# Optimization experiments

Hardware: AMD Instinct MI355X
Metric: run time of the kernel (lower is better)

The kernel has to match this reference:

```python
import jax, jax.numpy as jnp
import numpy as np

N_NODES = 100000
N_EDGES = 625000
D_IN = 128
D_OUT = 128


def setup_inputs() -> dict:
    key = jax.random.key(0)
    k1, k2, k3, k4, k5 = jax.random.split(key, 5)
    scale = 1.0 / np.sqrt(D_IN)
    x = jax.random.normal(k1, (N_NODES, D_IN), dtype=jnp.float32)
    edge_index = jax.random.randint(k2, (2, N_EDGES), 0, N_NODES, dtype=jnp.int64)
    W_l = jax.random.normal(k3, (D_IN, D_OUT), dtype=jnp.float32) * scale
    b_l = jax.random.normal(k4, (D_OUT,), dtype=jnp.float32) * scale
    W_r = jax.random.normal(k5, (D_IN, D_OUT), dtype=jnp.float32) * scale
    return {"x": x, "edge_index": edge_index, "W_l": W_l, "b_l": b_l, "W_r": W_r}


def reference(x, edge_index, W_l, b_l, W_r):
    # SAGEConv (mean aggr, no self loops):
    #   out = lin_l(mean_{j in N(i)} x_j) + lin_r(x_i)
    src = edge_index[0]  # message source nodes
    dst = edge_index[1]  # aggregation targets
    n = x.shape[0]
    msgs = x[src]  # [E, D_IN] gather
    agg = jax.ops.segment_sum(msgs, dst, num_segments=n)  # [N, D_IN]
    deg = jax.ops.segment_sum(jnp.ones_like(dst, dtype=x.dtype), dst, num_segments=n)
    mean = agg / jnp.maximum(deg, 1.0)[:, None]  # isolated nodes -> 0
    return mean @ W_l + b_l + x @ W_r
```

## Files before the change

### kernel.cpp

```cpp
#include <hip/hip_runtime.h>


constexpr int N_NODES = 100000;
constexpr int N_EDGES = 625000;
constexpr int D = 128;
constexpr int SCAN_CHUNK = 1024;
constexpr int N_SCAN_BLOCKS = (N_NODES + SCAN_CHUNK - 1) / SCAN_CHUNK;
constexpr int CONV_BLOCKS = N_NODES * D / (512 * 4);
constexpr int ZERO_BLOCKS = (N_NODES / 4 + 255) / 256;
constexpr int E4 = N_EDGES / 4;

typedef __attribute__((ext_vector_type(8))) short short8;
typedef __attribute__((ext_vector_type(4))) short short4v;
typedef __attribute__((ext_vector_type(4))) float f32x4;

__device__ __forceinline__ unsigned short f2bf(float f) {
    union { float f; unsigned int u; } c; c.f = f;
    unsigned int u = c.u + 0x7fffu + ((c.u >> 16) & 1u);
    return (unsigned short)(u >> 16);
}
__device__ __forceinline__ float bflo(unsigned int v) {
    union { unsigned int u; float f; } c; c.u = v << 16; return c.f;
}
__device__ __forceinline__ float bfhi(unsigned int v) {
    union { unsigned int u; float f; } c; c.u = v & 0xffff0000u; return c.f;
}
__device__ __forceinline__ uint2 pack4(float4 a) {
    uint2 r;
    r.x = (unsigned)f2bf(a.x) | ((unsigned)f2bf(a.y) << 16);
    r.y = (unsigned)f2bf(a.z) | ((unsigned)f2bf(a.w) << 16);
    return r;
}

__global__ __launch_bounds__(256) void prep_w(
    const float* __restrict__ Wl, const float* __restrict__ Wr,
    unsigned short* __restrict__ wT)
{
    int flat = blockIdx.x * 256 + threadIdx.x;
    int k  = flat >> 4;
    int n0 = (flat & 15) * 8;
    const float* Wsrc = (k < 128) ? &Wl[k * 128 + n0] : &Wr[(k - 128) * 128 + n0];
    float4 a = *(const float4*)Wsrc;
    float4 b = *(const float4*)(Wsrc + 4);
    wT[(n0 + 0) * 256 + k] = f2bf(a.x);
    wT[(n0 + 1) * 256 + k] = f2bf(a.y);
    wT[(n0 + 2) * 256 + k] = f2bf(a.z);
    wT[(n0 + 3) * 256 + k] = f2bf(a.w);
    wT[(n0 + 4) * 256 + k] = f2bf(b.x);
    wT[(n0 + 5) * 256 + k] = f2bf(b.y);
    wT[(n0 + 6) * 256 + k] = f2bf(b.z);
    wT[(n0 + 7) * 256 + k] = f2bf(b.w);
}

__global__ __launch_bounds__(256) void conv_x(
    const float* __restrict__ x, unsigned short* __restrict__ xb,
    int* __restrict__ cnt)
{
    const int tid = threadIdx.x;
    if (blockIdx.x < CONV_BLOCKS) {
        __shared__ uint2 ls[512];
        const float4* xp = (const float4*)x;
        const int base = blockIdx.x * 512;
        float4 v0 = xp[base + tid];
        float4 v1 = xp[base + 256 + tid];
        ls[tid]       = pack4(v0);
        ls[tid + 256] = pack4(v1);
        __syncthreads();
        uint4 q = ((const uint4*)ls)[tid];
        ((uint4*)xb)[base / 2 + tid] = q;
    } else {
        int t3 = (blockIdx.x - CONV_BLOCKS) * 256 + tid;
        if (t3 < N_NODES / 4) ((uint4*)cnt)[t3] = make_uint4(0, 0, 0, 0);
    }
}

__global__ __launch_bounds__(256) void hist4(
    const int* __restrict__ dst, int* __restrict__ cnt)
{
    int t = blockIdx.x * 256 + threadIdx.x;
    if (t < E4) {
        int e = t * 4;
        int4 d4 = *(const int4*)&dst[e];
        atomicAdd(&cnt[d4.x], 1);
        atomicAdd(&cnt[d4.y], 1);
        atomicAdd(&cnt[d4.z], 1);
        atomicAdd(&cnt[d4.w], 1);
    }
}

__global__ __launch_bounds__(256) void scan_blocks(
    const int* __restrict__ cnt, int* __restrict__ ptr, int* __restrict__ bsums)
{
    __shared__ int sh[256];
    const int t = threadIdx.x;
    const int base = blockIdx.x * SCAN_CHUNK + t * 4;
    int v0 = (base + 0 < N_NODES) ? cnt[base + 0] : 0;
    int v1 = (base + 1 < N_NODES) ? cnt[base + 1] : 0;
    int v2 = (base + 2 < N_NODES) ? cnt[base + 2] : 0;
    int v3 = (base + 3 < N_NODES) ? cnt[base + 3] : 0;
    const int tsum = v0 + v1 + v2 + v3;
    sh[t] = tsum;
    __syncthreads();
    #pragma unroll
    for (int off = 1; off < 256; off <<= 1) {
        int val = (t >= off) ? sh[t - off] : 0;
        __syncthreads();
        sh[t] += val;
        __syncthreads();
    }
    const int texcl = sh[t] - tsum;
    if (t == 255) bsums[blockIdx.x] = sh[255];
    int e0 = texcl, e1 = e0 + v0, e2 = e1 + v1, e3 = e2 + v2;
    if (base + 0 < N_NODES) ptr[base + 0] = e0;
    if (base + 1 < N_NODES) ptr[base + 1] = e1;
    if (base + 2 < N_NODES) ptr[base + 2] = e2;
    if (base + 3 < N_NODES) ptr[base + 3] = e3;
}

__global__ __launch_bounds__(256) void add_offsets_fused(
    int* __restrict__ ptr, int* __restrict__ cursor, const int* __restrict__ bsums)
{
    __shared__ int sh[256];
    const int t = threadIdx.x;
    int v = (t < blockIdx.x) ? bsums[t] : 0;
    sh[t] = v;
    __syncthreads();
    #pragma unroll
    for (int off = 128; off > 0; off >>= 1) {
        if (t < off) sh[t] += sh[t + off];
        __syncthreads();
    }
    const int soff = sh[0];
    const int base = blockIdx.x * SCAN_CHUNK + t * 4;
    #pragma unroll
    for (int j = 0; j < 4; ++j) {
        int i = base + j;
        if (i < N_NODES) {
            int p = ptr[i] + soff;
            ptr[i] = p;
            cursor[i] = p;
        }
    }
    if (blockIdx.x == 0 && t == 0) ptr[N_NODES] = N_EDGES;
}

__global__ __launch_bounds__(256) void csr_fill(
    const int* __restrict__ src, const int* __restrict__ dst,
    int* __restrict__ cursor, int* __restrict__ sorted_src)
{
    int t = blockIdx.x * 256 + threadIdx.x;
    if (t < E4) {
        int e = t * 4;
        int4 d4 = *(const int4*)&dst[e];
        int4 s4 = *(const int4*)&src[e];
        int p0 = atomicAdd(&cursor[d4.x], 1);
        int p1 = atomicAdd(&cursor[d4.y], 1);
        int p2 = atomicAdd(&cursor[d4.z], 1);
        int p3 = atomicAdd(&cursor[d4.w], 1);
        sorted_src[p0] = s4.x;
        sorted_src[p1] = s4.y;
        sorted_src[p2] = s4.z;
        sorted_src[p3] = s4.w;
    }
}

template<bool MBF>
__global__ __launch_bounds__(256) void sage_aggregate_bf(
    const unsigned short* __restrict__ xb,
    const int* __restrict__ ptr,
    const int* __restrict__ sorted_src,
    unsigned short* __restrict__ mean_bf,
    float* __restrict__ mean_f32)
{
    const int node = blockIdx.x * 16 + (threadIdx.x >> 4);
    if (node >= N_NODES) return;
    const int l = threadIdx.x & 15;
    const int beg = ptr[node];
    const int end = ptr[node + 1];
    const size_t off = (size_t)l * 8;

    float a0=0,a1=0,a2=0,a3=0,a4=0,a5=0,a6=0,a7=0;
    float b0=0,b1=0,b2=0,b3=0,b4=0,b5=0,b6=0,b7=0;
    float c0=0,c1=0,c2=0,c3=0,c4=0,c5=0,c6=0,c7=0;
    float d0=0,d1=0,d2=0,d3=0,d4=0,d5=0,d6=0,d7=0;

    for (int i = beg; i < end; i += 4) {
        int last = end - 1;
        int e1 = i + 1 < end ? i + 1 : last;
        int e2 = i + 2 < end ? i + 2 : last;
        int e3 = i + 3 < end ? i + 3 : last;
        float w1 = (i + 1 < end) ? 1.f : 0.f;
        float w2 = (i + 2 < end) ? 1.f : 0.f;
        float w3 = (i + 3 < end) ? 1.f : 0.f;
        int s0 = sorted_src[i],  s1 = sorted_src[e1];
        int s2 = sorted_src[e2], s3 = sorted_src[e3];
        uint4 v0 = *(const uint4*)&xb[(size_t)s0 * D + off];
        uint4 v1 = *(const uint4*)&xb[(size_t)s1 * D + off];
        uint4 v2 = *(const uint4*)&xb[(size_t)s2 * D + off];
        uint4 v3 = *(const uint4*)&xb[(size_t)s3 * D + off];
        a0+=bflo(v0.x); a1+=bfhi(v0.x); a2+=bflo(v0.y); a3+=bfhi(v0.y);
        a4+=bflo(v0.z); a5+=bfhi(v0.z); a6+=bflo(v0.w); a7+=bfhi(v0.w);
        b0=fmaf(w1,bflo(v1.x),b0); b1=fmaf(w1,bfhi(v1.x),b1);
        b2=fmaf(w1,bflo(v1.y),b2); b3=fmaf(w1,bfhi(v1.y),b3);
        b4=fmaf(w1,bflo(v1.z),b4); b5=fmaf(w1,bfhi(v1.z),b5);
        b6=fmaf(w1,bflo(v1.w),b6); b7=fmaf(w1,bfhi(v1.w),b7);
        c0=fmaf(w2,bflo(v2.x),c0); c1=fmaf(w2,bfhi(v2.x),c1);
        c2=fmaf(w2,bflo(v2.y),c2); c3=fmaf(w2,bfhi(v2.y),c3);
        c4=fmaf(w2,bflo(v2.z),c4); c5=fmaf(w2,bfhi(v2.z),c5);
        c6=fmaf(w2,bflo(v2.w),c6); c7=fmaf(w2,bfhi(v2.w),c7);
        d0=fmaf(w3,bflo(v3.x),d0); d1=fmaf(w3,bfhi(v3.x),d1);
        d2=fmaf(w3,bflo(v3.y),d2); d3=fmaf(w3,bfhi(v3.y),d3);
        d4=fmaf(w3,bflo(v3.z),d4); d5=fmaf(w3,bfhi(v3.z),d5);
        d6=fmaf(w3,bflo(v3.w),d6); d7=fmaf(w3,bfhi(v3.w),d7);
    }
    const float sc = 1.0f / fmaxf((float)(end - beg), 1.0f);
    float r0 = ((a0+b0)+(c0+d0))*sc, r1 = ((a1+b1)+(c1+d1))*sc;
    float r2 = ((a2+b2)+(c2+d2))*sc, r3 = ((a3+b3)+(c3+d3))*sc;
    float r4 = ((a4+b4)+(c4+d4))*sc, r5 = ((a5+b5)+(c5+d5))*sc;
    float r6 = ((a6+b6)+(c6+d6))*sc, r7 = ((a7+b7)+(c7+d7))*sc;

    if constexpr (MBF) {
        uint4 o;
        o.x = (unsigned)f2bf(r0) | ((unsigned)f2bf(r1) << 16);
        o.y = (unsigned)f2bf(r2) | ((unsigned)f2bf(r3) << 16);
        o.z = (unsigned)f2bf(r4) | ((unsigned)f2bf(r5) << 16);
        o.w = (unsigned)f2bf(r6) | ((unsigned)f2bf(r7) << 16);
        *(uint4*)&mean_bf[(size_t)node * D + off] = o;
    } else {
        *(float4*)&mean_f32[(size_t)node * D + off] = make_float4(r0, r1, r2, r3);
        *(float4*)&mean_f32[(size_t)node * D + off + 4] = make_float4(r4, r5, r6, r7);
    }
}

__global__ __launch_bounds__(256) void sage_gemm_rb(
    const unsigned short* __restrict__ xb,
    const unsigned short* __restrict__ mean_bf,
    const unsigned short* __restrict__ wT,
    const float* __restrict__ bl,
    float* __restrict__ out)
{
    __shared__ unsigned short sA[2][32 * 256];

    const int tid  = threadIdx.x;
    const int lane = tid & 63;
    const int w    = tid >> 6;
    const int l15  = lane & 15;
    const int lg   = lane >> 4;

    const int n0 = w * 32 + l15;
    const int n1 = n0 + 16;

    short8 B0[8], B1[8];
    #pragma unroll
    for (int s = 0; s < 8; ++s) {
        B0[s] = *(const short8*)&wT[(size_t)n0 * 256 + s * 32 + lg * 8];
        B1[s] = *(const short8*)&wT[(size_t)n1 * 256 + s * 32 + lg * 8];
    }

    const int a_r0 = l15;
    const int a_r1 = 16 + l15;
    const float bias0 = bl[n0];
    const float bias1 = bl[n1];

    const int nTiles = N_NODES / 32;

    auto stage = [&](int buf, int tile) {
        const int row0 = tile * 32;
        #pragma unroll
        for (int i = 0; i < 4; ++i) {
            int c = tid + i * 256;
            int r = c >> 5;
            int s = c & 31;
            const unsigned short* srcp = (s < 16)
                ? &mean_bf[(size_t)(row0 + r) * D + s * 8]
                : &xb[(size_t)(row0 + r) * D + (s - 16) * 8];
            short8 v = *(const short8*)srcp;
            *(short8*)&sA[buf][r * 256 + ((s ^ (r & 7)) << 3)] = v;
        }
    };

    int tile = blockIdx.x;
    if (tile < nTiles) stage(0, tile);
    int buf = 0;

    for (; tile < nTiles; tile += gridDim.x) {
        __syncthreads();
        int nxt = tile + gridDim.x;
        if (nxt < nTiles) stage(buf ^ 1, nxt);

        f32x4 acc00 = {0.f,0.f,0.f,0.f}, acc01 = {0.f,0.f,0.f,0.f};
        f32x4 acc10 = {0.f,0.f,0.f,0.f}, acc11 = {0.f,0.f,0.f,0.f};

        #pragma unroll
        for (int s = 0; s < 8; ++s) {
            int ks = s * 4 + lg;
            short8 a0 = *(const short8*)&sA[buf][a_r0 * 256 + ((ks ^ (a_r0 & 7)) << 3)];
            short8 a1 = *(const short8*)&sA[buf][a_r1 * 256 + ((ks ^ (a_r1 & 7)) << 3)];
            acc00 = __builtin_amdgcn_mfma_f32_16x16x32_bf16(a0, B0[s], acc00, 0, 0, 0);
            acc01 = __builtin_amdgcn_mfma_f32_16x16x32_bf16(a0, B1[s], acc01, 0, 0, 0);
            acc10 = __builtin_amdgcn_mfma_f32_16x16x32_bf16(a1, B0[s], acc10, 0, 0, 0);
            acc11 = __builtin_amdgcn_mfma_f32_16x16x32_bf16(a1, B1[s], acc11, 0, 0, 0);
        }

        const int row0 = tile * 32;
        #pragma unroll
        for (int reg = 0; reg < 4; ++reg) {
            int r0w = row0 + lg * 4 + reg;
            int r1w = r0w + 16;
            out[(size_t)r0w * D + n0] = acc00[reg] + bias0;
            out[(size_t)r0w * D + n1] = acc01[reg] + bias1;
            out[(size_t)r1w * D + n0] = acc10[reg] + bias0;
            out[(size_t)r1w * D + n1] = acc11[reg] + bias1;
        }
        buf ^= 1;
    }
}

__global__ __launch_bounds__(256) void wt_build(
    const float* __restrict__ Wl, const float* __restrict__ Wr,
    unsigned short* __restrict__ wT)
{
    int idx = blockIdx.x * 256 + threadIdx.x;
    if (idx >= 128 * 256) return;
    int n = idx >> 8;
    int k = idx & 255;
    float v = (k < 128) ? Wl[k * 128 + n] : Wr[(k - 128) * 128 + n];
    wT[n * 256 + k] = f2bf(v);
}

__global__ __launch_bounds__(256) void sage_aggregate(
    const float* __restrict__ x,
    const int* __restrict__ ptr,
    const int* __restrict__ sorted_src,
    float* __restrict__ mean)
{
    const int node = blockIdx.x * 4 + (threadIdx.x >> 6);
    if (node >= N_NODES) return;
    const int lane = threadIdx.x & 63;
    const int beg = ptr[node];
    const int end = ptr[node + 1];

    float2 acc0 = make_float2(0.f, 0.f);
    float2 acc1 = make_float2(0.f, 0.f);
    int i = beg;
    for (; i + 1 < end; i += 2) {
        int s0 = sorted_src[i];
        int s1 = sorted_src[i + 1];
        float2 a = *(const float2*)&x[(size_t)s0 * D + lane * 2];
        float2 b = *(const float2*)&x[(size_t)s1 * D + lane * 2];
        acc0.x += a.x; acc0.y += a.y;
        acc1.x += b.x; acc1.y += b.y;
    }
    if (i < end) {
        int s0 = sorted_src[i];
        float2 a = *(const float2*)&x[(size_t)s0 * D + lane * 2];
        acc0.x += a.x; acc0.y += a.y;
    }
    const float sc = 1.0f / fmaxf((float)(end - beg), 1.0f);
    float2 r = make_float2((acc0.x + acc1.x) * sc, (acc0.y + acc1.y) * sc);
    *(float2*)&mean[(size_t)node * D + lane * 2] = r;
}

__global__ __launch_bounds__(256) void sage_gemm_mfma(
    const float* __restrict__ x,
    const unsigned short* __restrict__ wT,
    const float* __restrict__ bl,
    float* __restrict__ out)
{
    __shared__ unsigned short sW[128 * 256];
    __shared__ unsigned short sA1[32 * 256];

    const int tid  = threadIdx.x;
    const int lane = tid & 63;
    const int w    = tid >> 6;
    const int l15  = lane & 15;
    const int lg   = lane >> 4;

    #pragma unroll
    for (int i = 0; i < 16; ++i) {
        int c  = tid + i * 256;
        int n  = c >> 5;
        int k8 = c & 31;
        short8 v = ((const short8*)wT)[c];
        *(short8*)&sW[n * 256 + ((k8 ^ (n & 7)) << 3)] = v;
    }

    const int a_r0 = l15;
    const int a_r1 = 16 + l15;
    const int n0 = w * 32 + l15;
    const int n1 = n0 + 16;
    const float bias0 = bl[n0];
    const float bias1 = bl[n1];
    const int nTiles = N_NODES / 32;

    for (int tile = blockIdx.x; tile < nTiles; tile += gridDim.x) {
        const int row0 = tile * 32;
        #pragma unroll
        for (int i = 0; i < 8; ++i) {
            int c    = tid + i * 256;
            int r    = c >> 6;
            int half = (c >> 5) & 1;
            int f4   = c & 31;
            const float* srcp = half ? &x[(size_t)(row0 + r) * D + f4 * 4]
                                     : &out[(size_t)(row0 + r) * D + f4 * 4];
            float4 v = *(const float4*)srcp;
            short4v b;
            b.x = (short)f2bf(v.x); b.y = (short)f2bf(v.y);
            b.z = (short)f2bf(v.z); b.w = (short)f2bf(v.w);
            int k = half * 128 + f4 * 4;
            int u = k >> 3;
            *(short4v*)&sA1[r * 256 + ((u ^ (r & 7)) << 3) + (k & 7)] = b;
        }
        __syncthreads();

        f32x4 acc00 = {0.f,0.f,0.f,0.f}, acc01 = {0.f,0.f,0.f,0.f};
        f32x4 acc10 = {0.f,0.f,0.f,0.f}, acc11 = {0.f,0.f,0.f,0.f};

        #pragma unroll
        for (int s = 0; s < 8; ++s) {
            int ks = s * 4 + lg;
            short8 a0 = *(const short8*)&sA1[a_r0 * 256 + ((ks ^ (a_r0 & 7)) << 3)];
            short8 a1 = *(const short8*)&sA1[a_r1 * 256 + ((ks ^ (a_r1 & 7)) << 3)];
            short8 b0 = *(const short8*)&sW[n0 * 256 + ((ks ^ (n0 & 7)) << 3)];
            short8 b1 = *(const short8*)&sW[n1 * 256 + ((ks ^ (n1 & 7)) << 3)];
            acc00 = __builtin_amdgcn_mfma_f32_16x16x32_bf16(a0, b0, acc00, 0, 0, 0);
            acc01 = __builtin_amdgcn_mfma_f32_16x16x32_bf16(a0, b1, acc01, 0, 0, 0);
            acc10 = __builtin_amdgcn_mfma_f32_16x16x32_bf16(a1, b0, acc10, 0, 0, 0);
            acc11 = __builtin_amdgcn_mfma_f32_16x16x32_bf16(a1, b1, acc11, 0, 0, 0);
        }
        __syncthreads();

        #pragma unroll
        for (int reg = 0; reg < 4; ++reg) {
            int r0w = row0 + lg * 4 + reg;
            int r1w = r0w + 16;
            out[(size_t)r0w * D + n0] = acc00[reg] + bias0;
            out[(size_t)r0w * D + n1] = acc01[reg] + bias1;
            out[(size_t)r1w * D + n0] = acc10[reg] + bias0;
            out[(size_t)r1w * D + n1] = acc11[reg] + bias1;
        }
    }
}

__global__ __launch_bounds__(256) void sage_scatter(
    const float* __restrict__ x, const int* __restrict__ src,
    const int* __restrict__ dst, float* __restrict__ agg, float* __restrict__ deg)
{
    int gid = blockIdx.x * 256 + threadIdx.x;
    int e = gid >> 7;
    if (e >= N_EDGES) return;
    int d = gid & 127;
    atomicAdd(&agg[(size_t)dst[e] * D + d], x[(size_t)src[e] * D + d]);
    if (d == 0) atomicAdd(&deg[dst[e]], 1.0f);
}

__global__ __launch_bounds__(256) void apply_mean(
    float* __restrict__ agg, const float* __restrict__ deg)
{
    int gid = blockIdx.x * 256 + threadIdx.x;
    int row = gid >> 5;
    if (row >= N_NODES) return;
    float sc = 1.0f / fmaxf(deg[row], 1.0f);
    float4 v = ((float4*)agg)[gid];
    v.x *= sc; v.y *= sc; v.z *= sc; v.w *= sc;
    ((float4*)agg)[gid] = v;
}

__device__ __forceinline__ void accum_tile(
    float acc[4][4], const float (*sWf)[D], const float (*srow)[D], int h, int j4)
{
    #pragma unroll 2
    for (int k = 0; k < D; k += 4) {
        float4 w0 = *(const float4*)&sWf[k + 0][j4];
        float4 w1 = *(const float4*)&sWf[k + 1][j4];
        float4 w2 = *(const float4*)&sWf[k + 2][j4];
        float4 w3 = *(const float4*)&sWf[k + 3][j4];
        #pragma unroll
        for (int r = 0; r < 4; ++r) {
            float4 a = *(const float4*)&srow[h + r * 8][k];
            acc[r][0] = fmaf(a.x, w0.x, fmaf(a.y, w1.x, fmaf(a.z, w2.x, fmaf(a.w, w3.x, acc[r][0]))));
            acc[r][1] = fmaf(a.x, w0.y, fmaf(a.y, w1.y, fmaf(a.z, w2.y, fmaf(a.w, w3.y, acc[r][1]))));
            acc[r][2] = fmaf(a.x, w0.z, fmaf(a.y, w1.z, fmaf(a.z, w2.z, fmaf(a.w, w3.z, acc[r][2]))));
            acc[r][3] = fmaf(a.x, w0.w, fmaf(a.y, w1.w, fmaf(a.z, w2.w, fmaf(a.w, w3.w, acc[r][3]))));
        }
    }
}

__global__ __launch_bounds__(256) void sage_gemm_f32(
    const float* __restrict__ x, const float* __restrict__ Wl,
    const float* __restrict__ bl, const float* __restrict__ Wr,
    float* __restrict__ out)
{
    __shared__ float sWf[D][D];
    __shared__ float srow[32][D];
    const int tid = threadIdx.x;
    const int j4 = (tid & 31) * 4;
    const int h  = tid >> 5;
    const int nTiles = (N_NODES + 31) / 32;
    const float4 bias = *(const float4*)(bl + j4);

    for (int tile = blockIdx.x; tile < nTiles; tile += gridDim.x) {
        const int row0 = tile * 32;
        float acc[4][4];
        #pragma unroll
        for (int r = 0; r < 4; ++r)
            #pragma unroll
            for (int c = 0; c < 4; ++c) acc[r][c] = 0.0f;

        __syncthreads();
        #pragma unroll
        for (int i = 0; i < 16; ++i)
            ((float4*)sWf)[tid + i * 256] = ((const float4*)Wl)[tid + i * 256];
        #pragma unroll
        for (int i = 0; i < 4; ++i) {
            int idx = tid + i * 256, r = idx >> 5, c = idx & 31, row = row0 + r;
            float4 v = make_float4(0.f,0.f,0.f,0.f);
            if (row < N_NODES) v = ((const float4*)out)[(size_t)row * 32 + c];
            ((float4*)srow)[idx] = v;
        }
        __syncthreads();
        accum_tile(acc, sWf, srow, h, j4);

        __syncthreads();
        #pragma unroll
        for (int i = 0; i < 16; ++i)
            ((float4*)sWf)[tid + i * 256] = ((const float4*)Wr)[tid + i * 256];
        #pragma unroll
        for (int i = 0; i < 4; ++i) {
            int idx = tid + i * 256, r = idx >> 5, c = idx & 31, row = row0 + r;
            float4 v = make_float4(0.f,0.f,0.f,0.f);
            if (row < N_NODES) v = ((const float4*)x)[(size_t)row * 32 + c];
            ((float4*)srow)[idx] = v;
        }
        __syncthreads();
        accum_tile(acc, sWf, srow, h, j4);

        #pragma unroll
        for (int r = 0; r < 4; ++r) {
            int row = row0 + h + r * 8;
            if (row < N_NODES) {
                float4 v = make_float4(acc[r][0] + bias.x, acc[r][1] + bias.y,
                                       acc[r][2] + bias.z, acc[r][3] + bias.w);
                *(float4*)(out + (size_t)row * D + j4) = v;
            }
        }
    }
}

extern "C" void kernel_launch(void* const* d_in, const int* in_sizes, int n_in,
                              void* d_out, int out_size, void* d_ws, size_t ws_size,
                              hipStream_t stream) {
    const float* x   = (const float*)d_in[0];
    const int*   ei  = (const int*)d_in[1];
    const float* Wl  = (const float*)d_in[2];
    const float* bl  = (const float*)d_in[3];
    const float* Wr  = (const float*)d_in[4];
    float* out = (float*)d_out;

    const int* src = ei;
    const int* dst = ei + N_EDGES;

    int* cnt    = (int*)d_ws;
    int* ptr    = cnt + N_NODES;
    int* cursor = ptr + N_NODES + 1;
    int* bsums  = cursor + N_NODES;
    int* sorted = bsums + 128;
    size_t int_count = (size_t)(3 * N_NODES + 1 + 128 + N_EDGES);
    int_count = (int_count + 7) & ~(size_t)7;
    unsigned short* wT      = (unsigned short*)((int*)d_ws + int_count);
    unsigned short* xb      = wT + 128 * 256;
    unsigned short* mean_bf = xb + (size_t)N_NODES * D;

    size_t need_B  = int_count * sizeof(int);
    size_t need_A  = need_B + 128 * 256 * 2 + 2 * (size_t)N_NODES * D * 2;

    if (ws_size >= need_A) {
        prep_w<<<16, 256, 0, stream>>>(Wl, Wr, wT);
        conv_x<<<CONV_BLOCKS + ZERO_BLOCKS, 256, 0, stream>>>(x, xb, cnt);
        hist4<<<(E4 + 255) / 256, 256, 0, stream>>>(dst, cnt);
        scan_blocks<<<N_SCAN_BLOCKS, 256, 0, stream>>>(cnt, ptr, bsums);
        add_offsets_fused<<<N_SCAN_BLOCKS, 256, 0, stream>>>(ptr, cursor, bsums);
        csr_fill<<<(E4 + 255) / 256, 256, 0, stream>>>(src, dst, cursor, sorted);
        sage_aggregate_bf<true><<<(N_NODES + 15) / 16, 256, 0, stream>>>(
            xb, ptr, sorted, mean_bf, nullptr);
        sage_gemm_rb<<<768, 256, 0, stream>>>(xb, mean_bf, wT, bl, out);
    } else if (ws_size >= need_B) {
        hipMemsetAsync(cnt, 0, (size_t)N_NODES * sizeof(int), stream);
        hist4<<<(E4 + 255) / 256, 256, 0, stream>>>(dst, cnt);
        scan_blocks<<<N_SCAN_BLOCKS, 256, 0, stream>>>(cnt, ptr, bsums);
        add_offsets_fused<<<N_SCAN_BLOCKS, 256, 0, stream>>>(ptr, cursor, bsums);
        csr_fill<<<(E4 + 255) / 256, 256, 0, stream>>>(src, dst, cursor, sorted);
        unsigned short* wTc = (unsigned short*)cursor;
        wt_build<<<(128 * 256 + 255) / 256, 256, 0, stream>>>(Wl, Wr, wTc);
        sage_aggregate<<<(N_NODES + 3) / 4, 256, 0, stream>>>(x, ptr, sorted, out);
        sage_gemm_mfma<<<512, 256, 0, stream>>>(x, wTc, bl, out);
    } else {
        float* deg = (float*)d_ws;
        hipMemsetAsync(out, 0, (size_t)N_NODES * D * sizeof(float), stream);
        hipMemsetAsync(deg, 0, (size_t)N_NODES * sizeof(float), stream);
        long long total = (long long)N_EDGES * 128;
        sage_scatter<<<(int)((total + 255) / 256), 256, 0, stream>>>(x, src, dst, out, deg);
        apply_mean<<<(N_NODES * 32 + 255) / 256, 256, 0, stream>>>(out, deg);
        sage_gemm_f32<<<512, 256, 0, stream>>>(x, Wl, bl, Wr, out);
    }
}
```

Measured before the change: 138.4 us.

## Fuse neighbor aggregation into MFMA GEMM and merge weight prep into conversion kernel

The mean-aggregation gather now writes its bf16 results straight into shared memory inside the GEMM kernel. This removes the mean_bf round trip through global memory and one kernel launch. The weight transpose/convert kernel is folded into the x-conversion kernel as extra blocks, saving another launch. The fused kernel uses one 32-row tile per block (3125 blocks) without double buffering. It reloads the B fragments in every block, and its MFMA work has to wait for the irregular gather latency.

```diff
diff --git a/kernel.cpp b/kernel.cpp
--- a/kernel.cpp
+++ b/kernel.cpp
@@ -32,28 +32,10 @@
     return r;
 }
 
-__global__ __launch_bounds__(256) void prep_w(
-    const float* __restrict__ Wl, const float* __restrict__ Wr,
-    unsigned short* __restrict__ wT)
-{
-    int flat = blockIdx.x * 256 + threadIdx.x;
-    int k  = flat >> 4;
-    int n0 = (flat & 15) * 8;
-    const float* Wsrc = (k < 128) ? &Wl[k * 128 + n0] : &Wr[(k - 128) * 128 + n0];
-    float4 a = *(const float4*)Wsrc;
-    float4 b = *(const float4*)(Wsrc + 4);
-    wT[(n0 + 0) * 256 + k] = f2bf(a.x);
-    wT[(n0 + 1) * 256 + k] = f2bf(a.y);
-    wT[(n0 + 2) * 256 + k] = f2bf(a.z);
-    wT[(n0 + 3) * 256 + k] = f2bf(a.w);
-    wT[(n0 + 4) * 256 + k] = f2bf(b.x);
-    wT[(n0 + 5) * 256 + k] = f2bf(b.y);
-    wT[(n0 + 6) * 256 + k] = f2bf(b.z);
-    wT[(n0 + 7) * 256 + k] = f2bf(b.w);
-}
-
-__global__ __launch_bounds__(256) void conv_x(
-    const float* __restrict__ x, unsigned short* __restrict__ xb,
+__global__ __launch_bounds__(256) void conv_all(
+    const float* __restrict__ x, const float* __restrict__ Wl,
+    const float* __restrict__ Wr,
+    unsigned short* __restrict__ xb, unsigned short* __restrict__ wT,
     int* __restrict__ cnt)
 {
     const int tid = threadIdx.x;
@@ -68,8 +50,23 @@
         __syncthreads();
         uint4 q = ((const uint4*)ls)[tid];
         ((uint4*)xb)[base / 2 + tid] = q;
+    } else if (blockIdx.x < CONV_BLOCKS + 16) {
+        int flat = (blockIdx.x - CONV_BLOCKS) * 256 + tid;
+        int k  = flat >> 4;
+        int n0 = (flat & 15) * 8;
+        const float* Wsrc = (k < 128) ? &Wl[k * 128 + n0] : &Wr[(k - 128) * 128 + n0];
+        float4 a = *(const float4*)Wsrc;
+        float4 b = *(const float4*)(Wsrc + 4);
+        wT[(n0 + 0) * 256 + k] = f2bf(a.x);
+        wT[(n0 + 1) * 256 + k] = f2bf(a.y);
+        wT[(n0 + 2) * 256 + k] = f2bf(a.z);
+        wT[(n0 + 3) * 256 + k] = f2bf(a.w);
+        wT[(n0 + 4) * 256 + k] = f2bf(b.x);
+        wT[(n0 + 5) * 256 + k] = f2bf(b.y);
+        wT[(n0 + 6) * 256 + k] = f2bf(b.z);
+        wT[(n0 + 7) * 256 + k] = f2bf(b.w);
     } else {
-        int t3 = (blockIdx.x - CONV_BLOCKS) * 256 + tid;
+        int t3 = (blockIdx.x - CONV_BLOCKS - 16) * 256 + tid;
         if (t3 < N_NODES / 4) ((uint4*)cnt)[t3] = make_uint4(0, 0, 0, 0);
     }
 }
@@ -164,82 +161,15 @@
     }
 }
 
-template<bool MBF>
-__global__ __launch_bounds__(256) void sage_aggregate_bf(
+__global__ __launch_bounds__(256) void sage_fused(
     const unsigned short* __restrict__ xb,
     const int* __restrict__ ptr,
     const int* __restrict__ sorted_src,
-    unsigned short* __restrict__ mean_bf,
-    float* __restrict__ mean_f32)
-{
-    const int node = blockIdx.x * 16 + (threadIdx.x >> 4);
-    if (node >= N_NODES) return;
-    const int l = threadIdx.x & 15;
-    const int beg = ptr[node];
-    const int end = ptr[node + 1];
-    const size_t off = (size_t)l * 8;
-
-    float a0=0,a1=0,a2=0,a3=0,a4=0,a5=0,a6=0,a7=0;
-    float b0=0,b1=0,b2=0,b3=0,b4=0,b5=0,b6=0,b7=0;
-    float c0=0,c1=0,c2=0,c3=0,c4=0,c5=0,c6=0,c7=0;
-    float d0=0,d1=0,d2=0,d3=0,d4=0,d5=0,d6=0,d7=0;
-
-    for (int i = beg; i < end; i += 4) {
-        int last = end - 1;
-        int e1 = i + 1 < end ? i + 1 : last;
-        int e2 = i + 2 < end ? i + 2 : last;
-        int e3 = i + 3 < end ? i + 3 : last;
-        float w1 = (i + 1 < end) ? 1.f : 0.f;
-        float w2 = (i + 2 < end) ? 1.f : 0.f;
-        float w3 = (i + 3 < end) ? 1.f : 0.f;
-        int s0 = sorted_src[i],  s1 = sorted_src[e1];
-        int s2 = sorted_src[e2], s3 = sorted_src[e3];
-        uint4 v0 = *(const uint4*)&xb[(size_t)s0 * D + off];
-        uint4 v1 = *(const uint4*)&xb[(size_t)s1 * D + off];
-        uint4 v2 = *(const uint4*)&xb[(size_t)s2 * D + off];
-        uint4 v3 = *(const uint4*)&xb[(size_t)s3 * D + off];
-        a0+=bflo(v0.x); a1+=bfhi(v0.x); a2+=bflo(v0.y); a3+=bfhi(v0.y);
-        a4+=bflo(v0.z); a5+=bfhi(v0.z); a6+=bflo(v0.w); a7+=bfhi(v0.w);
-        b0=fmaf(w1,bflo(v1.x),b0); b1=fmaf(w1,bfhi(v1.x),b1);
-        b2=fmaf(w1,bflo(v1.y),b2); b3=fmaf(w1,bfhi(v1.y),b3);
-        b4=fmaf(w1,bflo(v1.z),b4); b5=fmaf(w1,bfhi(v1.z),b5);
-        b6=fmaf(w1,bflo(v1.w),b6); b7=fmaf(w1,bfhi(v1.w),b7);
-        c0=fmaf(w2,bflo(v2.x),c0); c1=fmaf(w2,bfhi(v2.x),c1);
-        c2=fmaf(w2,bflo(v2.y),c2); c3=fmaf(w2,bfhi(v2.y),c3);
-        c4=fmaf(w2,bflo(v2.z),c4); c5=fmaf(w2,bfhi(v2.z),c5);
-        c6=fmaf(w2,bflo(v2.w),c6); c7=fmaf(w2,bfhi(v2.w),c7);
-        d0=fmaf(w3,bflo(v3.x),d0); d1=fmaf(w3,bfhi(v3.x),d1);
-        d2=fmaf(w3,bflo(v3.y),d2); d3=fmaf(w3,bfhi(v3.y),d3);
-        d4=fmaf(w3,bflo(v3.z),d4); d5=fmaf(w3,bfhi(v3.z),d5);
-        d6=fmaf(w3,bflo(v3.w),d6); d7=fmaf(w3,bfhi(v3.w),d7);
-    }
-    const float sc = 1.0f / fmaxf((float)(end - beg), 1.0f);
-    float r0 = ((a0+b0)+(c0+d0))*sc, r1 = ((a1+b1)+(c1+d1))*sc;
-    float r2 = ((a2+b2)+(c2+d2))*sc, r3 = ((a3+b3)+(c3+d3))*sc;
-    float r4 = ((a4+b4)+(c4+d4))*sc, r5 = ((a5+b5)+(c5+d5))*sc;
-    float r6 = ((a6+b6)+(c6+d6))*sc, r7 = ((a7+b7)+(c7+d7))*sc;
-
-    if constexpr (MBF) {
-        uint4 o;
-        o.x = (unsigned)f2bf(r0) | ((unsigned)f2bf(r1) << 16);
-        o.y = (unsigned)f2bf(r2) | ((unsigned)f2bf(r3) << 16);
-        o.z = (unsigned)f2bf(r4) | ((unsigned)f2bf(r5) << 16);
-        o.w = (unsigned)f2bf(r6) | ((unsigned)f2bf(r7) << 16);
-        *(uint4*)&mean_bf[(size_t)node * D + off] = o;
-    } else {
-        *(float4*)&mean_f32[(size_t)node * D + off] = make_float4(r0, r1, r2, r3);
-        *(float4*)&mean_f32[(size_t)node * D + off + 4] = make_float4(r4, r5, r6, r7);
-    }
-}
-
-__global__ __launch_bounds__(256) void sage_gemm_rb(
-    const unsigned short* __restrict__ xb,
-    const unsigned short* __restrict__ mean_bf,
     const unsigned short* __restrict__ wT,
     const float* __restrict__ bl,
     float* __restrict__ out)
 {
-    __shared__ unsigned short sA[2][32 * 256];
+    __shared__ unsigned short sA[32 * 256];
 
     const int tid  = threadIdx.x;
     const int lane = tid & 63;
@@ -256,63 +186,100 @@
         B0[s] = *(const short8*)&wT[(size_t)n0 * 256 + s * 32 + lg * 8];
         B1[s] = *(const short8*)&wT[(size_t)n1 * 256 + s * 32 + lg * 8];
     }
+    const float bias0 = bl[n0];
+    const float bias1 = bl[n1];
+
+    const int row0 = blockIdx.x * 32;
+
+    #pragma unroll
+    for (int i = 0; i < 2; ++i) {
+        int c = tid + i * 256;
+        int r = c >> 4;
+        int s = 16 + (c & 15);
+        short8 v = *(const short8*)&xb[(size_t)(row0 + r) * D + (c & 15) * 8];
+        *(short8*)&sA[r * 256 + ((s ^ (r & 7)) << 3)] = v;
+    }
+
+    {
+        const int g = tid >> 4;
+        const int l = tid & 15;
+        const size_t off = (size_t)l * 8;
+
+        auto gather_row = [&](int r) {
+            const int node = row0 + r;
+            const int beg = ptr[node];
+            const int end = ptr[node + 1];
+            float a0=0,a1=0,a2=0,a3=0,a4=0,a5=0,a6=0,a7=0;
+            float b0=0,b1=0,b2=0,b3=0,b4=0,b5=0,b6=0,b7=0;
+            float c0=0,c1=0,c2=0,c3=0,c4=0,c5=0,c6=0,c7=0;
+            float d0=0,d1=0,d2=0,d3=0,d4=0,d5=0,d6=0,d7=0;
+            for (int i = beg; i < end; i += 4) {
+                int last = end - 1;
+                int e1 = i + 1 < end ? i + 1 : last;
+                int e2 = i + 2 < end ? i + 2 : last;
+                int e3 = i + 3 < end ? i + 3 : last;
+                float w1 = (i + 1 < end) ? 1.f : 0.f;
+                float w2 = (i + 2 < end) ? 1.f : 0.f;
+                float w3 = (i + 3 < end) ? 1.f : 0.f;
+                int s0 = sorted_src[i],  s1 = sorted_src[e1];
+                int s2 = sorted_src[e2], s3 = sorted_src[e3];
+                uint4 v0 = *(const uint4*)&xb[(size_t)s0 * D + off];
+                uint4 v1 = *(const uint4*)&xb[(size_t)s1 * D + off];
+                uint4 v2 = *(const uint4*)&xb[(size_t)s2 * D + off];
+                uint4 v3 = *(const uint4*)&xb[(size_t)s3 * D + off];
+                a0+=bflo(v0.x); a1+=bfhi(v0.x); a2+=bflo(v0.y); a3+=bfhi(v0.y);
+                a4+=bflo(v0.z); a5+=bfhi(v0.z); a6+=bflo(v0.w); a7+=bfhi(v0.w);
+                b0=fmaf(w1,bflo(v1.x),b0); b1=fmaf(w1,bfhi(v1.x),b1);
+                b2=fmaf(w1,bflo(v1.y),b2); b3=fmaf(w1,bfhi(v1.y),b3);
+                b4=fmaf(w1,bflo(v1.z),b4); b5=fmaf(w1,bfhi(v1.z),b5);
+                b6=fmaf(w1,bflo(v1.w),b6); b7=fmaf(w1,bfhi(v1.w),b7);
+                c0=fmaf(w2,bflo(v2.x),c0); c1=fmaf(w2,bfhi(v2.x),c1);
+                c2=fmaf(w2,bflo(v2.y),c2); c3=fmaf(w2,bfhi(v2.y),c3);
+                c4=fmaf(w2,bflo(v2.z),c4); c5=fmaf(w2,bfhi(v2.z),c5);
+                c6=fmaf(w2,bflo(v2.w),c6); c7=fmaf(w2,bfhi(v2.w),c7);
+                d0=fmaf(w3,bflo(v3.x),d0); d1=fmaf(w3,bfhi(v3.x),d1);
+                d2=fmaf(w3,bflo(v3.y),d2); d3=fmaf(w3,bfhi(v3.y),d3);
+                d4=fmaf(w3,bflo(v3.z),d4); d5=fmaf(w3,bfhi(v3.z),d5);
+                d6=fmaf(w3,bflo(v3.w),d6); d7=fmaf(w3,bfhi(v3.w),d7);
+            }
+            const float sc = 1.0f / fmaxf((float)(end - beg), 1.0f);
+            uint4 o;
+            o.x = (unsigned)f2bf(((a0+b0)+(c0+d0))*sc) | ((unsigned)f2bf(((a1+b1)+(c1+d1))*sc) << 16);
+            o.y = (unsigned)f2bf(((a2+b2)+(c2+d2))*sc) | ((unsigned)f2bf(((a3+b3)+(c3+d3))*sc) << 16);
+            o.z = (unsigned)f2bf(((a4+b4)+(c4+d4))*sc) | ((unsigned)f2bf(((a5+b5)+(c5+d5))*sc) << 16);
+            o.w = (unsigned)f2bf(((a6+b6)+(c6+d6))*sc) | ((unsigned)f2bf(((a7+b7)+(c7+d7))*sc) << 16);
+            *(uint4*)&sA[r * 256 + ((l ^ (r & 7)) << 3)] = o;
+        };
+        gather_row(g);
+        gather_row(g + 16);
+    }
+    __syncthreads();
 
     const int a_r0 = l15;
     const int a_r1 = 16 + l15;
-    const float bias0 = bl[n0];
-    const float bias1 = bl[n1];
-
-    const int nTiles = N_NODES / 32;
-
-    auto stage = [&](int buf, int tile) {
-        const int row0 = tile * 32;
-        #pragma unroll
-        for (int i = 0; i < 4; ++i) {
-            int c = tid + i * 256;
-            int r = c >> 5;
-            int s = c & 31;
-            const unsigned short* srcp = (s < 16)
-                ? &mean_bf[(size_t)(row0 + r) * D + s * 8]
-                : &xb[(size_t)(row0 + r) * D + (s - 16) * 8];
-            short8 v = *(const short8*)srcp;
-            *(short8*)&sA[buf][r * 256 + ((s ^ (r & 7)) << 3)] = v;
-        }
-    };
-
-    int tile = blockIdx.x;
-    if (tile < nTiles) stage(0, tile);
-    int buf = 0;
-
-    for (; tile < nTiles; tile += gridDim.x) {
-        __syncthreads();
-        int nxt = tile + gridDim.x;
-        if (nxt < nTiles) stage(buf ^ 1, nxt);
-
-        f32x4 acc00 = {0.f,0.f,0.f,0.f}, acc01 = {0.f,0.f,0.f,0.f};
-        f32x4 acc10 = {0.f,0.f,0.f,0.f}, acc11 = {0.f,0.f,0.f,0.f};
-
-        #pragma unroll
-        for (int s = 0; s < 8; ++s) {
-            int ks = s * 4 + lg;
-            short8 a0 = *(const short8*)&sA[buf][a_r0 * 256 + ((ks ^ (a_r0 & 7)) << 3)];
-            short8 a1 = *(const short8*)&sA[buf][a_r1 * 256 + ((ks ^ (a_r1 & 7)) << 3)];
-            acc00 = __builtin_amdgcn_mfma_f32_16x16x32_bf16(a0, B0[s], acc00, 0, 0, 0);
-            acc01 = __builtin_amdgcn_mfma_f32_16x16x32_bf16(a0, B1[s], acc01, 0, 0, 0);
-            acc10 = __builtin_amdgcn_mfma_f32_16x16x32_bf16(a1, B0[s], acc10, 0, 0, 0);
-            acc11 = __builtin_amdgcn_mfma_f32_16x16x32_bf16(a1, B1[s], acc11, 0, 0, 0);
-        }
-
-        const int row0 = tile * 32;
-        #pragma unroll
-        for (int reg = 0; reg < 4; ++reg) {
-            int r0w = row0 + lg * 4 + reg;
-            int r1w = r0w + 16;
-            out[(size_t)r0w * D + n0] = acc00[reg] + bias0;
-            out[(size_t)r0w * D + n1] = acc01[reg] + bias1;
-            out[(size_t)r1w * D + n0] = acc10[reg] + bias0;
-            out[(size_t)r1w * D + n1] = acc11[reg] + bias1;
-        }
-        buf ^= 1;
+
+    f32x4 acc00 = {0.f,0.f,0.f,0.f}, acc01 = {0.f,0.f,0.f,0.f};
+    f32x4 acc10 = {0.f,0.f,0.f,0.f}, acc11 = {0.f,0.f,0.f,0.f};
+
+    #pragma unroll
+    for (int s = 0; s < 8; ++s) {
+        int ks = s * 4 + lg;
+        short8 a0 = *(const short8*)&sA[a_r0 * 256 + ((ks ^ (a_r0 & 7)) << 3)];
+        short8 a1 = *(const short8*)&sA[a_r1 * 256 + ((ks ^ (a_r1 & 7)) << 3)];
+        acc00 = __builtin_amdgcn_mfma_f32_16x16x32_bf16(a0, B0[s], acc00, 0, 0, 0);
+        acc01 = __builtin_amdgcn_mfma_f32_16x16x32_bf16(a0, B1[s], acc01, 0, 0, 0);
+        acc10 = __builtin_amdgcn_mfma_f32_16x16x32_bf16(a1, B0[s], acc10, 0, 0, 0);
+        acc11 = __builtin_amdgcn_mfma_f32_16x16x32_bf16(a1, B1[s], acc11, 0, 0, 0);
+    }
+
+    #pragma unroll
+    for (int reg = 0; reg < 4; ++reg) {
+        int r0w = row0 + lg * 4 + reg;
+        int r1w = r0w + 16;
+        out[(size_t)r0w * D + n0] = acc00[reg] + bias0;
+        out[(size_t)r0w * D + n1] = acc01[reg] + bias1;
+        out[(size_t)r1w * D + n0] = acc10[reg] + bias0;
+        out[(size_t)r1w * D + n1] = acc11[reg] + bias1;
     }
 }
 
@@ -567,23 +534,20 @@
     int* sorted = bsums + 128;
     size_t int_count = (size_t)(3 * N_NODES + 1 + 128 + N_EDGES);
     int_count = (int_count + 7) & ~(size_t)7;
-    unsigned short* wT      = (unsigned short*)((int*)d_ws + int_count);
-    unsigned short* xb      = wT + 128 * 256;
-    unsigned short* mean_bf = xb + (size_t)N_NODES * D;
-
-    size_t need_B  = int_count * sizeof(int);
-    size_t need_A  = need_B + 128 * 256 * 2 + 2 * (size_t)N_NODES * D * 2;
+    unsigned short* wT = (unsigned short*)((int*)d_ws + int_count);
+    unsigned short* xb = wT + 128 * 256;
+
+    size_t need_B = int_count * sizeof(int);
+    size_t need_A = need_B + 128 * 256 * 2 + (size_t)N_NODES * D * 2;
 
     if (ws_size >= need_A) {
-        prep_w<<<16, 256, 0, stream>>>(Wl, Wr, wT);
-        conv_x<<<CONV_BLOCKS + ZERO_BLOCKS, 256, 0, stream>>>(x, xb, cnt);
+        conv_all<<<CONV_BLOCKS + 16 + ZERO_BLOCKS, 256, 0, stream>>>(
+            x, Wl, Wr, xb, wT, cnt);
         hist4<<<(E4 + 255) / 256, 256, 0, stream>>>(dst, cnt);
         scan_blocks<<<N_SCAN_BLOCKS, 256, 0, stream>>>(cnt, ptr, bsums);
         add_offsets_fused<<<N_SCAN_BLOCKS, 256, 0, stream>>>(ptr, cursor, bsums);
         csr_fill<<<(E4 + 255) / 256, 256, 0, stream>>>(src, dst, cursor, sorted);
-        sage_aggregate_bf<true><<<(N_NODES + 15) / 16, 256, 0, stream>>>(
-            xb, ptr, sorted, mean_bf, nullptr);
-        sage_gemm_rb<<<768, 256, 0, stream>>>(xb, mean_bf, wT, bl, out);
+        sage_fused<<<N_NODES / 32, 256, 0, stream>>>(xb, ptr, sorted, wT, bl, out);
     } else if (ws_size >= need_B) {
         hipMemsetAsync(cnt, 0, (size_t)N_NODES * sizeof(int), stream);
         hist4<<<(E4 + 255) / 256, 256, 0, stream>>>(dst, cnt);
```

Result: no change. 139.5 us (+0.8%).
